# Optimization experiments

Hardware: AMD Instinct MI355X
Metric: run time of the kernel (lower is better)

## Reference

```python
import jax, jax.numpy as jnp
import numpy as np

B, L, DH = 8, 512, 768
D_ARC, D_REL, C = 512, 128, 37


def setup_inputs() -> dict:
    key = jax.random.key(0)
    ks = jax.random.split(key, 14)
    n = jax.random.normal
    return {
        "H": n(ks[0], (B, L, DH), jnp.float32),
        "W_ah": n(ks[1], (D_ARC, DH), jnp.float32) * 0.02,
        "b_ah": n(ks[2], (D_ARC,), jnp.float32) * 0.02,
        "W_ad": n(ks[3], (D_ARC, DH), jnp.float32) * 0.02,
        "b_ad": n(ks[4], (D_ARC,), jnp.float32) * 0.02,
        "W_arc": n(ks[5], (D_ARC, D_ARC), jnp.float32) * 0.02,
        "bias_arc": n(ks[6], (D_ARC,), jnp.float32) * 0.02,
        "W_rh": n(ks[7], (D_REL, DH), jnp.float32) * 0.02,
        "b_rh": n(ks[8], (D_REL,), jnp.float32) * 0.02,
        "W_rd": n(ks[9], (D_REL, DH), jnp.float32) * 0.02,
        "b_rd": n(ks[10], (D_REL,), jnp.float32) * 0.02,
        "U_rel": n(ks[11], (C, D_REL, D_REL), jnp.float32) * 0.02,
        "W_rel": n(ks[12], (C, 2 * D_REL), jnp.float32) * 0.02,
        "bias_rel": n(ks[13], (C,), jnp.float32) * 0.02,
    }


def reference(H, W_ah, b_ah, W_ad, b_ad, W_arc, bias_arc,
              W_rh, b_rh, W_rd, b_rd, U_rel, W_rel, bias_rel):
    relu = jax.nn.relu
    # Arc path: MLPs (dropout is identity at inference)
    Hah = relu(H @ W_ah.T + b_ah)          # [B,L,d_arc] heads
    Had = relu(H @ W_ad.T + b_ad)          # [B,L,d_arc] deps
    # S_arc[b,l,m] = (Had W_arc^T)[b,l] . Hah[b,m] + Hah[b,l] . bias_arc
    S_arc = jnp.einsum('bld,bmd->blm', Had @ W_arc.T, Hah)
    S_arc = S_arc + (Hah @ bias_arc)[:, :, None]
    # Rel path
    Hrh = relu(H @ W_rh.T + b_rh)          # [B,L,d_rel]
    Hrd = relu(H @ W_rd.T + b_rd)          # [B,L,d_rel]
    # Bilinear per-label term: [B,L,L,C]
    bilin = jnp.einsum('bld,cde,bme->blmc', Hrh, U_rel, Hrd)
    # Affine term: faithful to the original expand — both head and dep are
    # taken at index l (expansion over dim 2), so it is independent of m.
    affine = jnp.concatenate([Hrh, Hrd], axis=-1) @ W_rel.T  # [B,L,C]
    S_rel = bilin + affine[:, :, None, :] + bias_rel
    return (S_arc, S_rel)
```

## Files before the change

### kernel.cpp

```cpp
#include <hip/hip_runtime.h>
#include <hip/hip_bf16.h>

typedef __attribute__((ext_vector_type(8))) short bf16x8;
typedef __attribute__((ext_vector_type(4))) float f32x4;

#define DEVINL __device__ __forceinline__

constexpr int kB = 8, kL = 512, kDH = 768, kDARC = 512, kDREL = 128, kC = 37;
constexpr int kBL = kB * kL;
constexpr int kNP = 1280;
constexpr int kNY = kC * kDREL;

constexpr long nHB   = (long)kBL * kDH;
constexpr long nWALL = (long)kNP * kDH;
constexpr long nWARC = (long)kDARC * kDARC;
constexpr long nUT   = (long)kC * kDREL * kDREL;
constexpr long nBALL = kNP;

DEVINL short f2b(float f) {
  unsigned u = __float_as_uint(f);
  u += 0x7fffu + ((u >> 16) & 1u);
  return (short)(u >> 16);
}
DEVINL float b2f(short s) {
  return __uint_as_float(((unsigned)(unsigned short)s) << 16);
}

DEVINL void gload16(const void* g, void* l) {
  __builtin_amdgcn_global_load_lds(
      (const __attribute__((address_space(1))) void*)g,
      (__attribute__((address_space(3))) void*)l, 16, 0, 0);
}

DEVINL void lds_barrier() {
  asm volatile("s_waitcnt lgkmcnt(0)\n\ts_barrier" ::: "memory");
}

__global__ __launch_bounds__(256) void k_convert(
    const float* __restrict__ H, const float* __restrict__ W_ah, const float* __restrict__ b_ah,
    const float* __restrict__ W_ad, const float* __restrict__ b_ad,
    const float* __restrict__ W_arc, const float* __restrict__ W_rh, const float* __restrict__ b_rh,
    const float* __restrict__ W_rd, const float* __restrict__ b_rd, const float* __restrict__ U,
    short* __restrict__ Hb, short* __restrict__ Wall, float* __restrict__ ballf,
    short* __restrict__ Warcb, short* __restrict__ Ut)
{
  const long total = nHB + nWALL + nWARC + nUT + nBALL;
  for (long i = (long)blockIdx.x * blockDim.x + threadIdx.x; i < total;
       i += (long)gridDim.x * blockDim.x) {
    if (i < nHB) {
      Hb[i] = f2b(H[i]);
    } else if (i < nHB + nWALL) {
      long j = i - nHB; int row = (int)(j / kDH); int k = (int)(j - (long)row * kDH);
      float v;
      if (row < 512)       v = W_ah[(long)row * kDH + k];
      else if (row < 1024) v = W_ad[(long)(row - 512) * kDH + k];
      else if (row < 1152) v = W_rh[(long)(row - 1024) * kDH + k];
      else                 v = W_rd[(long)(row - 1152) * kDH + k];
      Wall[j] = f2b(v);
    } else if (i < nHB + nWALL + nWARC) {
      long j = i - nHB - nWALL;
      Warcb[j] = f2b(W_arc[j]);
    } else if (i < nHB + nWALL + nWARC + nUT) {
      long j = i - nHB - nWALL - nWARC;
      int c = (int)(j >> 14); int rem = (int)(j & 16383); int e = rem >> 7; int d = rem & 127;
      Ut[j] = f2b(U[(long)c * 16384 + (long)d * 128 + e]);
    } else {
      int n = (int)(i - nHB - nWALL - nWARC - nUT);
      float v;
      if (n < 512)       v = b_ah[n];
      else if (n < 1024) v = b_ad[n - 512];
      else if (n < 1152) v = b_rh[n - 1024];
      else               v = b_rd[n - 1152];
      ballf[n] = v;
    }
  }
}

DEVINL void gemm128_core(short* As, short* Bs,
                         const short* __restrict__ Ag, long lda,
                         const short* __restrict__ Bg, long ldb,
                         int K, f32x4 acc[4][4])
{
  const int t = threadIdx.x, lane = t & 63, w = t >> 6;
  const int wm = w >> 1, wn = w & 1, fr = lane & 15, hi = lane >> 4;
  const int srow = w * 8 + (lane >> 3);
  const int scol = (lane & 7) * 8;
  const short* Arow = Ag + (long)srow * lda + scol;
  const short* Brow = Bg + (long)srow * ldb + scol;

  for (int k0 = 0; k0 < K; k0 += 64) {
    __syncthreads();
#pragma unroll
    for (int i = 0; i < 4; i++) {
      gload16(Arow + (long)i * 32 * lda + k0, &As[(i * 4 + w) * 512]);
      gload16(Brow + (long)i * 32 * ldb + k0, &Bs[(i * 4 + w) * 512]);
    }
    __syncthreads();
#pragma unroll
    for (int ks = 0; ks < 2; ks++) {
      bf16x8 a[4], b[4];
#pragma unroll
      for (int mf = 0; mf < 4; mf++)
        a[mf] = *(const bf16x8*)&As[(wm * 64 + mf * 16 + fr) * 64 + ks * 32 + hi * 8];
#pragma unroll
      for (int nf = 0; nf < 4; nf++)
        b[nf] = *(const bf16x8*)&Bs[(wn * 64 + nf * 16 + fr) * 64 + ks * 32 + hi * 8];
#pragma unroll
      for (int mf = 0; mf < 4; mf++)
#pragma unroll
        for (int nf = 0; nf < 4; nf++)
          acc[mf][nf] = __builtin_amdgcn_mfma_f32_16x16x32_bf16(a[mf], b[nf], acc[mf][nf], 0, 0, 0);
    }
  }
}

#define ZERO_ACC16 \
  f32x4 acc[4][4]; \
  for (int i = 0; i < 4; i++) for (int j = 0; j < 4; j++) for (int r = 0; r < 4; r++) acc[i][j][r] = 0.f;

__global__ __launch_bounds__(256) void k_proj(const short* __restrict__ Hb,
    const short* __restrict__ Wall, const float* __restrict__ ballf,
    short* __restrict__ Proj)
{
  __shared__ short As[128 * 64], Bs[128 * 64];
  const int tn = blockIdx.x, tm = blockIdx.y;
  ZERO_ACC16;
  gemm128_core(As, Bs, Hb + (long)tm * 128 * kDH, kDH, Wall + (long)tn * 128 * kDH, kDH, kDH, acc);
  const int lane = threadIdx.x & 63; const int w = threadIdx.x >> 6;
  const int wm = w >> 1, wn = w & 1, fr = lane & 15, hi = lane >> 4;
  for (int mf = 0; mf < 4; mf++) for (int nf = 0; nf < 4; nf++) for (int r = 0; r < 4; r++) {
    int row = tm * 128 + wm * 64 + mf * 16 + hi * 4 + r;
    int col = tn * 128 + wn * 64 + nf * 16 + fr;
    float v = acc[mf][nf][r] + ballf[col];
    v = v > 0.f ? v : 0.f;
    Proj[(long)row * kNP + col] = f2b(v);
  }
}

__global__ __launch_bounds__(256) void k_mid(const short* __restrict__ Proj,
    const short* __restrict__ Warcb, const short* __restrict__ Ut,
    const float* __restrict__ bias_arc, const float* __restrict__ W_rel,
    const float* __restrict__ bias_rel,
    short* __restrict__ T, short* __restrict__ Y,
    float* __restrict__ rowterm, float* __restrict__ affB)
{
  __shared__ short As[128 * 64], Bs[128 * 64];
  const int bx = blockIdx.x;
  const int t = threadIdx.x;

  if (bx < 1312) {
    const short* Ag; const short* Bg;
    long lda, ldb, ldd; int K, tm, tn; short* dst;
    if (bx < 128) {
      tn = bx & 3; tm = bx >> 2;
      Ag = Proj + (long)tm * 128 * kNP + 512; lda = kNP;
      Bg = Warcb + (long)tn * 128 * kDARC;    ldb = kDARC;
      K = kDARC; dst = T; ldd = kDARC;
    } else {
      int i = bx - 128; tn = i % 37; tm = i / 37;
      Ag = Proj + (long)tm * 128 * kNP + 1024; lda = kNP;
      Bg = Ut + (long)tn * 128 * kDREL;        ldb = kDREL;
      K = kDREL; dst = Y; ldd = kNY;
    }
    ZERO_ACC16;
    gemm128_core(As, Bs, Ag, lda, Bg, ldb, K, acc);
    const int lane = t & 63; const int w = t >> 6;
    const int wm = w >> 1, wn = w & 1, fr = lane & 15, hi = lane >> 4;
    for (int mf = 0; mf < 4; mf++) for (int nf = 0; nf < 4; nf++) for (int r = 0; r < 4; r++) {
      int row = tm * 128 + wm * 64 + mf * 16 + hi * 4 + r;
      int col = tn * 128 + wn * 64 + nf * 16 + fr;
      dst[(long)row * ldd + col] = f2b(acc[mf][nf][r]);
    }
  } else {
    __shared__ float h[4][256];
    const int base = (bx - 1312) * 8;
    const int w = t >> 6, lane = t & 63;
    for (int j = 0; j < 2; j++) {
      const int bl = base + w * 2 + j;
      const short* prow = Proj + (long)bl * kNP;
      float s = 0.f;
      bf16x8 hv = *(const bf16x8*)(prow + lane * 8);
#pragma unroll
      for (int i = 0; i < 8; i++) s += b2f(hv[i]) * bias_arc[lane * 8 + i];
      for (int off = 32; off; off >>= 1) s += __shfl_down(s, off, 64);
      if (lane == 0) rowterm[bl] = s;
      if (lane < 32) {
        bf16x8 v = *(const bf16x8*)(prow + 1024 + lane * 8);
        for (int i = 0; i < 8; i++) h[w][lane * 8 + i] = b2f(v[i]);
      }
      __syncthreads();
      if (lane < kC) {
        float sa = bias_rel[lane];
        const float* wr = W_rel + (long)lane * 256;
        for (int k = 0; k < 256; k++) sa += h[w][k] * wr[k];
        affB[(long)bl * kC + lane] = sa;
      }
      __syncthreads();
    }
  }
}

__global__ __launch_bounds__(256) void k_out(const short* __restrict__ T,
    const short* __restrict__ Proj, const float* __restrict__ rowterm,
    const short* __restrict__ Y, const float* __restrict__ affB,
    float* __restrict__ outArc, float* __restrict__ outRel)
{
  extern __shared__ short sm[];
  const int t = threadIdx.x;
  const int lane = t & 63, w = t >> 6;
  const int fr = lane & 15, hi = lane >> 4;

  if (blockIdx.x < 128) {
    const int i = blockIdx.x;
    const int b = i >> 4, tm = (i >> 2) & 3, tn = i & 3;
    ZERO_ACC16;
    gemm128_core(sm, sm + 8192,
                 T + ((long)b * kL + tm * 128) * kDARC, kDARC,
                 Proj + ((long)b * kL + tn * 128) * kNP, kNP, kDARC, acc);
    const int wm = w >> 1, wn = w & 1;
    for (int mf = 0; mf < 4; mf++) for (int nf = 0; nf < 4; nf++) for (int r = 0; r < 4; r++) {
      int l = tm * 128 + wm * 64 + mf * 16 + hi * 4 + r;
      int m = tn * 128 + wn * 64 + nf * 16 + fr;
      outArc[((long)b * kL + l) * kL + m] = acc[mf][nf][r] + rowterm[(long)b * kL + l];
    }
  } else {
    const int idx = blockIdx.x - 128;
    const int h = idx & 1;
    const int l0 = ((idx >> 1) & 63) * 8;
    const int b = idx >> 7;
    const int mbase = h * 256;
    short* Bcur = sm;
    short* Bnxt = sm + 6528;
    float* scrBase = (float*)(sm + 13056);

    bf16x8 a[4][4];
    const short* Ab = Proj + ((long)b * kL + mbase + w * 64) * kNP + 1152;
#pragma unroll
    for (int mf = 0; mf < 4; mf++)
#pragma unroll
      for (int ks = 0; ks < 4; ks++)
        a[mf][ks] = *(const bf16x8*)(Ab + (long)(mf * 16 + fr) * kNP + ks * 32 + hi * 8);

    {
      const short* Yrow = Y + ((long)b * kL + l0) * kNY;
#pragma unroll
      for (int p = 0; p < 3; p++) {
        int i2 = p * 256 + t;
        if (i2 < 592)
          *(bf16x8*)&Bcur[(i2 >> 4) * 136 + (i2 & 15) * 8] = *(const bf16x8*)(Yrow + i2 * 8);
      }
    }
    lds_barrier();

    for (int il = 0; il < 8; il++) {
      const long bl = (long)b * kL + l0 + il;

      bf16x8 n0, n1, n2;
      if (il < 7) {
        const short* Yn = Y + (bl + 1) * kNY;
        n0 = *(const bf16x8*)(Yn + t * 8);
        n1 = *(const bf16x8*)(Yn + (long)(256 + t) * 8);
        if (t < 80) n2 = *(const bf16x8*)(Yn + (long)(512 + t) * 8);
      }

      f32x4 acc[3][4];
#pragma unroll
      for (int cf = 0; cf < 3; cf++)
#pragma unroll
        for (int mf = 0; mf < 4; mf++)
          for (int r = 0; r < 4; r++) acc[cf][mf][r] = 0.f;

#pragma unroll
      for (int ks = 0; ks < 4; ks++) {
        bf16x8 yfr[3];
#pragma unroll
        for (int cf = 0; cf < 3; cf++)
          yfr[cf] = *(const bf16x8*)&Bcur[(cf * 16 + fr) * 136 + ks * 32 + hi * 8];
#pragma unroll
        for (int cf = 0; cf < 3; cf++)
#pragma unroll
          for (int mf = 0; mf < 4; mf++)
            acc[cf][mf] = __builtin_amdgcn_mfma_f32_16x16x32_bf16(yfr[cf], a[mf][ks], acc[cf][mf], 0, 0, 0);
      }

      if (il < 7) {
        *(bf16x8*)&Bnxt[(t >> 4) * 136 + (t & 15) * 8] = n0;
        {
          int i2 = 256 + t;
          *(bf16x8*)&Bnxt[(i2 >> 4) * 136 + (i2 & 15) * 8] = n1;
        }
        if (t < 80) {
          int i2 = 512 + t;
          *(bf16x8*)&Bnxt[(i2 >> 4) * 136 + (i2 & 15) * 8] = n2;
        }
        lds_barrier();
        short* tmp = Bcur; Bcur = Bnxt; Bnxt = tmp;
      }

      const float* afb = affB + bl * kC;
      f32x4 aff0 = *(const f32x4*)&afb[hi * 4];
      f32x4 aff1 = *(const f32x4*)&afb[16 + hi * 4];
      f32x4 aff2 = (hi == 0) ? *(const f32x4*)&afb[32] : f32x4{0.f, 0.f, 0.f, 0.f};
      float aff36 = afb[36];

      float* scr = scrBase + w * 592;
#pragma unroll
      for (int mf = 0; mf < 4; mf++) {
        f32x4 v0 = acc[0][mf] + aff0;
        f32x4 v1 = acc[1][mf] + aff1;
        *(f32x4*)&scr[fr * 37 + hi * 4] = v0;
        *(f32x4*)&scr[fr * 37 + 16 + hi * 4] = v1;
        if (hi == 0) {
          f32x4 v2 = acc[2][mf] + aff2;
          *(f32x4*)&scr[fr * 37 + 32] = v2;
        } else if (hi == 1) {
          scr[fr * 37 + 36] = acc[2][mf][0] + aff36;
        }
        float* gb = outRel + (bl * kL + mbase + w * 64 + mf * 16) * kC;
#pragma unroll
        for (int p = 0; p < 3; p++) {
          int i4 = p * 64 + lane;
          if (i4 < 148) {
            f32x4 v = *(f32x4*)&scr[i4 * 4];
            *(f32x4*)&gb[i4 * 4] = v;
          }
        }
      }
    }
  }
}

extern "C" void kernel_launch(void* const* d_in, const int* in_sizes, int n_in,
                              void* d_out, int out_size, void* d_ws, size_t ws_size,
                              hipStream_t stream) {
  const float* H        = (const float*)d_in[0];
  const float* W_ah     = (const float*)d_in[1];
  const float* b_ah     = (const float*)d_in[2];
  const float* W_ad     = (const float*)d_in[3];
  const float* b_ad     = (const float*)d_in[4];
  const float* W_arc    = (const float*)d_in[5];
  const float* bias_arc = (const float*)d_in[6];
  const float* W_rh     = (const float*)d_in[7];
  const float* b_rh     = (const float*)d_in[8];
  const float* W_rd     = (const float*)d_in[9];
  const float* b_rd     = (const float*)d_in[10];
  const float* U_rel    = (const float*)d_in[11];
  const float* W_rel    = (const float*)d_in[12];
  const float* bias_rel = (const float*)d_in[13];

  size_t off = 0;
  auto take = [&](size_t nbytes) -> void* {
    void* p = (char*)d_ws + off;
    off += (nbytes + 255) & ~(size_t)255;
    return p;
  };
  short* Hb      = (short*)take(nHB * 2);
  short* Wall    = (short*)take(nWALL * 2);
  float* ballf   = (float*)take(nBALL * 4);
  short* Warcb   = (short*)take(nWARC * 2);
  short* Ut      = (short*)take(nUT * 2);
  short* Proj    = (short*)take((long)kBL * kNP * 2);
  short* T       = (short*)take((long)kBL * kDARC * 2);
  short* Y       = (short*)take((long)kBL * kNY * 2);
  float* rowterm = (float*)take((long)kBL * 4);
  float* affB    = (float*)take((long)kBL * kC * 4);
  if (off > ws_size) return;

  float* outArc = (float*)d_out;
  float* outRel = outArc + (long)kB * kL * kL;

  k_convert<<<dim3(2048), dim3(256), 0, stream>>>(H, W_ah, b_ah, W_ad, b_ad, W_arc,
                                                  W_rh, b_rh, W_rd, b_rd, U_rel,
                                                  Hb, Wall, ballf, Warcb, Ut);
  k_proj<<<dim3(kNP / 128, kBL / 128), dim3(256), 0, stream>>>(Hb, Wall, ballf, Proj);
  k_mid<<<dim3(1824), dim3(256), 0, stream>>>(Proj, Warcb, Ut, bias_arc, W_rel, bias_rel,
                                              T, Y, rowterm, affB);
  k_out<<<dim3(1152), dim3(256), 35584, stream>>>(T, Proj, rowterm, Y, affB, outArc, outRel);
}
```

Baseline: 169.3 us.

## Pad Y rows to LDS layout, stream with async global-to-LDS loads, split output kernel

The mid kernel now writes Y in a padded row layout (stride 136 per label) that matches the LDS tile, so the relation-output kernel can fetch each next row with direct global_load_lds DMA instead of register staging and LDS stores. The bilinear output is written straight from accumulators to global memory, dropping the LDS scratch transpose. The arc and relation output paths are split into two separate kernels, with the relation kernel launched first. In exchange the stores are less coalesced and there is one more kernel launch, and each barrier now also waits on outstanding vector memory operations.

```diff
diff --git a/kernel.cpp b/kernel.cpp
--- a/kernel.cpp
+++ b/kernel.cpp
@@ -9,7 +9,7 @@
 constexpr int kB = 8, kL = 512, kDH = 768, kDARC = 512, kDREL = 128, kC = 37;
 constexpr int kBL = kB * kL;
 constexpr int kNP = 1280;
-constexpr int kNY = kC * kDREL;
+constexpr int kYR = 5032;
 
 constexpr long nHB   = (long)kBL * kDH;
 constexpr long nWALL = (long)kNP * kDH;
@@ -32,8 +32,8 @@
       (__attribute__((address_space(3))) void*)l, 16, 0, 0);
 }
 
-DEVINL void lds_barrier() {
-  asm volatile("s_waitcnt lgkmcnt(0)\n\ts_barrier" ::: "memory");
+DEVINL void vm_lds_barrier() {
+  asm volatile("s_waitcnt vmcnt(0) lgkmcnt(0)\n\ts_barrier" ::: "memory");
 }
 
 __global__ __launch_bounds__(256) void k_convert(
@@ -141,7 +141,7 @@
     const short* __restrict__ Warcb, const short* __restrict__ Ut,
     const float* __restrict__ bias_arc, const float* __restrict__ W_rel,
     const float* __restrict__ bias_rel,
-    short* __restrict__ T, short* __restrict__ Y,
+    short* __restrict__ T, short* __restrict__ Ypad,
     float* __restrict__ rowterm, float* __restrict__ affB)
 {
   __shared__ short As[128 * 64], Bs[128 * 64];
@@ -150,26 +150,35 @@
 
   if (bx < 1312) {
     const short* Ag; const short* Bg;
-    long lda, ldb, ldd; int K, tm, tn; short* dst;
-    if (bx < 128) {
+    long lda, ldb; int K, tm, tn;
+    const bool isT = bx < 128;
+    if (isT) {
       tn = bx & 3; tm = bx >> 2;
       Ag = Proj + (long)tm * 128 * kNP + 512; lda = kNP;
       Bg = Warcb + (long)tn * 128 * kDARC;    ldb = kDARC;
-      K = kDARC; dst = T; ldd = kDARC;
+      K = kDARC;
     } else {
       int i = bx - 128; tn = i % 37; tm = i / 37;
       Ag = Proj + (long)tm * 128 * kNP + 1024; lda = kNP;
       Bg = Ut + (long)tn * 128 * kDREL;        ldb = kDREL;
-      K = kDREL; dst = Y; ldd = kNY;
+      K = kDREL;
     }
     ZERO_ACC16;
     gemm128_core(As, Bs, Ag, lda, Bg, ldb, K, acc);
     const int lane = t & 63; const int w = t >> 6;
     const int wm = w >> 1, wn = w & 1, fr = lane & 15, hi = lane >> 4;
-    for (int mf = 0; mf < 4; mf++) for (int nf = 0; nf < 4; nf++) for (int r = 0; r < 4; r++) {
-      int row = tm * 128 + wm * 64 + mf * 16 + hi * 4 + r;
-      int col = tn * 128 + wn * 64 + nf * 16 + fr;
-      dst[(long)row * ldd + col] = f2b(acc[mf][nf][r]);
+    if (isT) {
+      for (int mf = 0; mf < 4; mf++) for (int nf = 0; nf < 4; nf++) for (int r = 0; r < 4; r++) {
+        int row = tm * 128 + wm * 64 + mf * 16 + hi * 4 + r;
+        int col = tn * 128 + wn * 64 + nf * 16 + fr;
+        T[(long)row * kDARC + col] = f2b(acc[mf][nf][r]);
+      }
+    } else {
+      for (int mf = 0; mf < 4; mf++) for (int nf = 0; nf < 4; nf++) for (int r = 0; r < 4; r++) {
+        int row = tm * 128 + wm * 64 + mf * 16 + hi * 4 + r;
+        int e = wn * 64 + nf * 16 + fr;
+        Ypad[(long)row * kYR + tn * 136 + e] = f2b(acc[mf][nf][r]);
+      }
     }
   } else {
     __shared__ float h[4][256];
@@ -200,132 +209,117 @@
   }
 }
 
-__global__ __launch_bounds__(256) void k_out(const short* __restrict__ T,
+__global__ __launch_bounds__(256) void k_sarc(const short* __restrict__ T,
     const short* __restrict__ Proj, const float* __restrict__ rowterm,
-    const short* __restrict__ Y, const float* __restrict__ affB,
-    float* __restrict__ outArc, float* __restrict__ outRel)
-{
-  extern __shared__ short sm[];
+    float* __restrict__ outArc)
+{
+  __shared__ short As[128 * 64], Bs[128 * 64];
+  const int i = blockIdx.x;
+  const int b = i >> 4, tm = (i >> 2) & 3, tn = i & 3;
+  ZERO_ACC16;
+  gemm128_core(As, Bs,
+               T + ((long)b * kL + tm * 128) * kDARC, kDARC,
+               Proj + ((long)b * kL + tn * 128) * kNP, kNP, kDARC, acc);
+  const int lane = threadIdx.x & 63; const int w = threadIdx.x >> 6;
+  const int wm = w >> 1, wn = w & 1, fr = lane & 15, hi = lane >> 4;
+  for (int mf = 0; mf < 4; mf++) for (int nf = 0; nf < 4; nf++) for (int r = 0; r < 4; r++) {
+    int l = tm * 128 + wm * 64 + mf * 16 + hi * 4 + r;
+    int m = tn * 128 + wn * 64 + nf * 16 + fr;
+    outArc[((long)b * kL + l) * kL + m] = acc[mf][nf][r] + rowterm[(long)b * kL + l];
+  }
+}
+
+__global__ __launch_bounds__(256) void k_srel(const short* __restrict__ Proj,
+    const short* __restrict__ Ypad, const float* __restrict__ affB,
+    float* __restrict__ outRel)
+{
+  __shared__ short Bbuf[2][48 * 136];
   const int t = threadIdx.x;
   const int lane = t & 63, w = t >> 6;
   const int fr = lane & 15, hi = lane >> 4;
-
-  if (blockIdx.x < 128) {
-    const int i = blockIdx.x;
-    const int b = i >> 4, tm = (i >> 2) & 3, tn = i & 3;
-    ZERO_ACC16;
-    gemm128_core(sm, sm + 8192,
-                 T + ((long)b * kL + tm * 128) * kDARC, kDARC,
-                 Proj + ((long)b * kL + tn * 128) * kNP, kNP, kDARC, acc);
-    const int wm = w >> 1, wn = w & 1;
-    for (int mf = 0; mf < 4; mf++) for (int nf = 0; nf < 4; nf++) for (int r = 0; r < 4; r++) {
-      int l = tm * 128 + wm * 64 + mf * 16 + hi * 4 + r;
-      int m = tn * 128 + wn * 64 + nf * 16 + fr;
-      outArc[((long)b * kL + l) * kL + m] = acc[mf][nf][r] + rowterm[(long)b * kL + l];
-    }
-  } else {
-    const int idx = blockIdx.x - 128;
-    const int h = idx & 1;
-    const int l0 = ((idx >> 1) & 63) * 8;
-    const int b = idx >> 7;
-    const int mbase = h * 256;
-    short* Bcur = sm;
-    short* Bnxt = sm + 6528;
-    float* scrBase = (float*)(sm + 13056);
-
-    bf16x8 a[4][4];
-    const short* Ab = Proj + ((long)b * kL + mbase + w * 64) * kNP + 1152;
-#pragma unroll
-    for (int mf = 0; mf < 4; mf++)
-#pragma unroll
-      for (int ks = 0; ks < 4; ks++)
-        a[mf][ks] = *(const bf16x8*)(Ab + (long)(mf * 16 + fr) * kNP + ks * 32 + hi * 8);
-
-    {
-      const short* Yrow = Y + ((long)b * kL + l0) * kNY;
-#pragma unroll
-      for (int p = 0; p < 3; p++) {
-        int i2 = p * 256 + t;
-        if (i2 < 592)
-          *(bf16x8*)&Bcur[(i2 >> 4) * 136 + (i2 & 15) * 8] = *(const bf16x8*)(Yrow + i2 * 8);
-      }
-    }
-    lds_barrier();
-
-    for (int il = 0; il < 8; il++) {
-      const long bl = (long)b * kL + l0 + il;
-
-      bf16x8 n0, n1, n2;
-      if (il < 7) {
-        const short* Yn = Y + (bl + 1) * kNY;
-        n0 = *(const bf16x8*)(Yn + t * 8);
-        n1 = *(const bf16x8*)(Yn + (long)(256 + t) * 8);
-        if (t < 80) n2 = *(const bf16x8*)(Yn + (long)(512 + t) * 8);
-      }
-
-      f32x4 acc[3][4];
+  const int idx = blockIdx.x;
+  const int h = idx & 1;
+  const int l0 = ((idx >> 1) & 63) * 8;
+  const int b = idx >> 7;
+  const int mbase = h * 256;
+
+  bf16x8 a[4][4];
+  const short* Ab = Proj + ((long)b * kL + mbase + w * 64) * kNP + 1152;
+#pragma unroll
+  for (int mf = 0; mf < 4; mf++)
+#pragma unroll
+    for (int ks = 0; ks < 4; ks++)
+      a[mf][ks] = *(const bf16x8*)(Ab + (long)(mf * 16 + fr) * kNP + ks * 32 + hi * 8);
+
+  const char* Ybase = (const char*)(Ypad + (long)(b * kL + l0) * kYR);
+
+#pragma unroll
+  for (int i = 0; i < 3; i++) {
+    int ii = w + i * 4;
+    if (ii < 10) {
+      int off = ii * 1024;
+      if (off + lane * 16 < 10064)
+        gload16(Ybase + off + lane * 16, (char*)Bbuf[0] + off);
+    }
+  }
+  vm_lds_barrier();
+
+  int cur = 0;
+  for (int il = 0; il < 8; il++) {
+    const long bl = (long)b * kL + l0 + il;
+
+    if (il < 7) {
+      const char* Yn = Ybase + (long)(il + 1) * kYR * 2;
+#pragma unroll
+      for (int i = 0; i < 3; i++) {
+        int ii = w + i * 4;
+        if (ii < 10) {
+          int off = ii * 1024;
+          if (off + lane * 16 < 10064)
+            gload16(Yn + off + lane * 16, (char*)Bbuf[cur ^ 1] + off);
+        }
+      }
+    }
+
+    f32x4 acc[3][4];
+#pragma unroll
+    for (int cf = 0; cf < 3; cf++)
+#pragma unroll
+      for (int mf = 0; mf < 4; mf++)
+        for (int r = 0; r < 4; r++) acc[cf][mf][r] = 0.f;
+
+#pragma unroll
+    for (int ks = 0; ks < 4; ks++) {
+      bf16x8 yfr[3];
 #pragma unroll
       for (int cf = 0; cf < 3; cf++)
+        yfr[cf] = *(const bf16x8*)&Bbuf[cur][(cf * 16 + fr) * 136 + ks * 32 + hi * 8];
+#pragma unroll
+      for (int cf = 0; cf < 3; cf++)
 #pragma unroll
         for (int mf = 0; mf < 4; mf++)
-          for (int r = 0; r < 4; r++) acc[cf][mf][r] = 0.f;
-
-#pragma unroll
-      for (int ks = 0; ks < 4; ks++) {
-        bf16x8 yfr[3];
-#pragma unroll
-        for (int cf = 0; cf < 3; cf++)
-          yfr[cf] = *(const bf16x8*)&Bcur[(cf * 16 + fr) * 136 + ks * 32 + hi * 8];
-#pragma unroll
-        for (int cf = 0; cf < 3; cf++)
-#pragma unroll
-          for (int mf = 0; mf < 4; mf++)
-            acc[cf][mf] = __builtin_amdgcn_mfma_f32_16x16x32_bf16(yfr[cf], a[mf][ks], acc[cf][mf], 0, 0, 0);
-      }
-
-      if (il < 7) {
-        *(bf16x8*)&Bnxt[(t >> 4) * 136 + (t & 15) * 8] = n0;
-        {
-          int i2 = 256 + t;
-          *(bf16x8*)&Bnxt[(i2 >> 4) * 136 + (i2 & 15) * 8] = n1;
-        }
-        if (t < 80) {
-          int i2 = 512 + t;
-          *(bf16x8*)&Bnxt[(i2 >> 4) * 136 + (i2 & 15) * 8] = n2;
-        }
-        lds_barrier();
-        short* tmp = Bcur; Bcur = Bnxt; Bnxt = tmp;
-      }
-
-      const float* afb = affB + bl * kC;
-      f32x4 aff0 = *(const f32x4*)&afb[hi * 4];
-      f32x4 aff1 = *(const f32x4*)&afb[16 + hi * 4];
-      f32x4 aff2 = (hi == 0) ? *(const f32x4*)&afb[32] : f32x4{0.f, 0.f, 0.f, 0.f};
-      float aff36 = afb[36];
-
-      float* scr = scrBase + w * 592;
-#pragma unroll
-      for (int mf = 0; mf < 4; mf++) {
-        f32x4 v0 = acc[0][mf] + aff0;
-        f32x4 v1 = acc[1][mf] + aff1;
-        *(f32x4*)&scr[fr * 37 + hi * 4] = v0;
-        *(f32x4*)&scr[fr * 37 + 16 + hi * 4] = v1;
-        if (hi == 0) {
-          f32x4 v2 = acc[2][mf] + aff2;
-          *(f32x4*)&scr[fr * 37 + 32] = v2;
-        } else if (hi == 1) {
-          scr[fr * 37 + 36] = acc[2][mf][0] + aff36;
-        }
-        float* gb = outRel + (bl * kL + mbase + w * 64 + mf * 16) * kC;
-#pragma unroll
-        for (int p = 0; p < 3; p++) {
-          int i4 = p * 64 + lane;
-          if (i4 < 148) {
-            f32x4 v = *(f32x4*)&scr[i4 * 4];
-            *(f32x4*)&gb[i4 * 4] = v;
-          }
-        }
-      }
+          acc[cf][mf] = __builtin_amdgcn_mfma_f32_16x16x32_bf16(yfr[cf], a[mf][ks], acc[cf][mf], 0, 0, 0);
+    }
+
+    const float* afb = affB + bl * kC;
+    f32x4 aff0 = *(const f32x4*)&afb[hi * 4];
+    f32x4 aff1 = *(const f32x4*)&afb[16 + hi * 4];
+
+    for (int mf = 0; mf < 4; mf++) {
+      float* gb = outRel + (bl * kL + mbase + w * 64 + mf * 16 + fr) * kC;
+      *(f32x4*)&gb[hi * 4] = acc[0][mf] + aff0;
+      *(f32x4*)&gb[16 + hi * 4] = acc[1][mf] + aff1;
+      if (hi == 0) {
+        f32x4 v2 = acc[2][mf] + *(const f32x4*)&afb[32];
+        *(f32x4*)&gb[32] = v2;
+      } else if (hi == 1) {
+        gb[36] = acc[2][mf][0] + afb[36];
+      }
+    }
+
+    if (il < 7) {
+      vm_lds_barrier();
+      cur ^= 1;
     }
   }
 }
@@ -361,7 +355,7 @@
   short* Ut      = (short*)take(nUT * 2);
   short* Proj    = (short*)take((long)kBL * kNP * 2);
   short* T       = (short*)take((long)kBL * kDARC * 2);
-  short* Y       = (short*)take((long)kBL * kNY * 2);
+  short* Ypad    = (short*)take((long)kBL * kYR * 2);
   float* rowterm = (float*)take((long)kBL * 4);
   float* affB    = (float*)take((long)kBL * kC * 4);
   if (off > ws_size) return;
@@ -374,6 +368,7 @@
                                                   Hb, Wall, ballf, Warcb, Ut);
   k_proj<<<dim3(kNP / 128, kBL / 128), dim3(256), 0, stream>>>(Hb, Wall, ballf, Proj);
   k_mid<<<dim3(1824), dim3(256), 0, stream>>>(Proj, Warcb, Ut, bias_arc, W_rel, bias_rel,
-                                              T, Y, rowterm, affB);
-  k_out<<<dim3(1152), dim3(256), 35584, stream>>>(T, Proj, rowterm, Y, affB, outArc, outRel);
-}
+                                              T, Ypad, rowterm, affB);
+  k_srel<<<dim3(1024), dim3(256), 0, stream>>>(Proj, Ypad, affB, outRel);
+  k_sarc<<<dim3(128), dim3(256), 0, stream>>>(T, Proj, rowterm, outArc);
+}
```

Result: slower. 180.6 us (+6.6%).
